# Optimization experiments

Measured on AMD Instinct MI355X. Metric: run time of the kernel, lower is better.

## Reference

```python
import jax, jax.numpy as jnp
import numpy as np

N, E, D, ED, SH = 100000, 1600000, 64, 16, 9

# Real spherical harmonics l=0,1,2, 'integral' normalization (e3nn default),
# applied to unit direction vectors. Coefficients: 1/(2*sqrt(pi)), sqrt(3/4pi), etc.

def _sh(d):
    x, y, z = d[:, 0], d[:, 1], d[:, 2]
    return jnp.stack([
        jnp.full_like(x, 0.28209479177387814),          # l=0
        0.4886025119029199 * y,                          # l=1, m=-1
        0.4886025119029199 * z,                          # l=1, m=0
        0.4886025119029199 * x,                          # l=1, m=1
        1.0925484305920792 * x * y,                      # l=2, m=-2
        1.0925484305920792 * y * z,                      # l=2, m=-1
        0.31539156525252005 * (3.0 * z * z - 1.0),       # l=2, m=0
        1.0925484305920792 * x * z,                      # l=2, m=1
        0.5462742152960396 * (x * x - y * y),            # l=2, m=2
    ], axis=1)


def _mlp(h, W1, b1, W2, b2):  # Linear -> SiLU -> Linear
    return jax.nn.silu(h @ W1 + b1) @ W2 + b2


def setup_inputs() -> dict:
    key = jax.random.key(0)
    ks = jax.random.split(key, 16)
    def rn(k, shape, scale=0.05):
        return jax.random.normal(k, shape, dtype=jnp.float32) * scale
    return {
        "x": jax.random.normal(ks[0], (N, D), jnp.float32),
        "pos": jax.random.normal(ks[1], (N, 3), jnp.float32) * 3.0,
        "edge_attr": jax.random.normal(ks[2], (E, ED), jnp.float32),
        "row": jax.random.randint(ks[3], (E,), 0, N, dtype=jnp.int32),
        "col": jax.random.randint(ks[4], (E,), 0, N, dtype=jnp.int32),
        "node_W1": rn(ks[5], (D, D)), "node_b1": jnp.zeros((D,), jnp.float32),
        "node_W2": rn(ks[6], (D, D)), "node_b2": jnp.zeros((D,), jnp.float32),
        "edge_W1": rn(ks[7], (SH + ED, D)), "edge_b1": jnp.zeros((D,), jnp.float32),
        "edge_W2": rn(ks[8], (D, D)), "edge_b2": jnp.zeros((D,), jnp.float32),
        "out_W1": rn(ks[9], (2 * D, D)), "out_b1": jnp.zeros((D,), jnp.float32),
        "out_W2": rn(ks[10], (D, D)), "out_b2": jnp.zeros((D,), jnp.float32),
        "bn_gamma": jnp.ones((D,), jnp.float32), "bn_beta": jnp.zeros((D,), jnp.float32),
    }


def reference(x, pos, edge_attr, row, col,
              node_W1, node_b1, node_W2, node_b2,
              edge_W1, edge_b1, edge_W2, edge_b2,
              out_W1, out_b1, out_W2, out_b2,
              bn_gamma, bn_beta):
    # gather node positions per edge -> relative vectors
    rel = pos[row] - pos[col]                                    # [E,3]
    length = jnp.sqrt(jnp.sum(rel * rel, axis=1, keepdims=True) + 1e-12)
    d = rel / length
    d = d / (jnp.sqrt(jnp.sum(d * d, axis=1, keepdims=True)) + 1e-10)
    edge_sh = _sh(d)                                             # [E,9]
    edge_feat = jnp.concatenate([edge_sh, edge_attr], axis=1)    # [E,9+ED]
    x_t = _mlp(x, node_W1, node_b1, node_W2, node_b2)            # [N,D]
    e_w = _mlp(edge_feat, edge_W1, edge_b1, edge_W2, edge_b2)    # [E,D]
    msg = x_t[row] * e_w                                         # message = x_j * edge_attr
    # scatter-mean onto target nodes (edge_index[1] == col)
    s = jax.ops.segment_sum(msg, col, num_segments=N)            # [N,D]
    cnt = jax.ops.segment_sum(jnp.ones((E,), msg.dtype), col, num_segments=N)
    agg = s / jnp.maximum(cnt, 1.0)[:, None]
    h = jnp.concatenate([agg, x], axis=1)                        # [N,2D]
    h = _mlp(h, out_W1, out_b1, out_W2, out_b2)                  # [N,D]
    # BatchNorm over node dim (scalar irreps), training-mode batch stats
    mean = jnp.mean(h, axis=0)
    var = jnp.var(h, axis=0)
    return (h - mean) / jnp.sqrt(var + 1e-5) * bn_gamma + bn_beta
```

## Files before the change

### kernel.cpp

```cpp
#include <hip/hip_runtime.h>
#include <math.h>

#define DD 64
#define EDA 16

#define FR_E1 0
#define FR_E2 4
#define FR_N1 12
#define FR_N2 20
#define FR_O1 28
#define FR_O2 44
#define FR_TOT 52

#define PADH 72
#define PADF 68

#define HS 72

typedef unsigned int u32;
typedef unsigned long long u64;
typedef __attribute__((ext_vector_type(8))) short short8;
typedef __attribute__((ext_vector_type(4))) float f32x4;

static __device__ __forceinline__ float silu(float v) {
    return v / (1.0f + __expf(-v));
}
static __device__ __forceinline__ unsigned short f2bf(float f) {
    unsigned u = __float_as_uint(f);
    unsigned r = u + 0x7FFFu + ((u >> 16) & 1u);
    return (unsigned short)(r >> 16);
}
static __device__ __forceinline__ float bf2f(unsigned short u) {
    return __uint_as_float(((unsigned)u) << 16);
}
static __device__ __forceinline__ float bflo(u32 v) {
    return __uint_as_float(v << 16);
}
static __device__ __forceinline__ float bfhi(u32 v) {
    return __uint_as_float(v & 0xFFFF0000u);
}
static __device__ __forceinline__ unsigned cvt_pk_bf16(float lo, float hi) {
    unsigned r;
    asm("v_cvt_pk_bf16_f32 %0, %1, %2" : "=v"(r) : "v"(lo), "v"(hi));
    return r;
}
static __device__ __forceinline__ int bperm(int idx_lane, int v) {
    return __builtin_amdgcn_ds_bpermute(idx_lane << 2, v);
}
static __device__ __forceinline__ void wave_lds_fence() {
    asm volatile("s_waitcnt lgkmcnt(0)" ::: "memory");
    __builtin_amdgcn_sched_barrier(0);
}

__global__ __launch_bounds__(256) void k_pack_zero(
    const float* __restrict__ eW1, const float* __restrict__ eW2,
    const float* __restrict__ nW1, const float* __restrict__ nW2,
    const float* __restrict__ oW1, const float* __restrict__ oW2,
    unsigned short* __restrict__ wpk,
    uint4* __restrict__ zbase, int nz4)
{
    if (blockIdx.x > 0) {
        int i = (blockIdx.x - 1) * 256 + threadIdx.x;
        if (i < nz4) zbase[i] = make_uint4(0u, 0u, 0u, 0u);
        return;
    }
    int t = threadIdx.x;
    int nt = t >> 6, l = t & 63;
    int kc = l >> 4, n0 = l & 15;

    #pragma unroll
    for (int j = 0; j < 8; ++j) {
        int k = kc*8 + j;
        int orig = (k < 16) ? (9 + k) : ((k < 25) ? (k - 16) : -1);
        float v = (orig >= 0) ? eW1[orig*DD + nt*16 + n0] : 0.0f;
        wpk[((size_t)((FR_E1 + nt)*64 + l))*8 + j] = f2bf(v);
    }
    #pragma unroll
    for (int s = 0; s < 2; ++s) {
        #pragma unroll
        for (int j = 0; j < 8; ++j) {
            int k = s*32 + kc*8 + j;
            wpk[((size_t)((FR_E2 + s*4 + nt)*64 + l))*8 + j] = f2bf(eW2[k*DD + nt*16 + n0]);
            wpk[((size_t)((FR_N1 + s*4 + nt)*64 + l))*8 + j] = f2bf(nW1[k*DD + nt*16 + n0]);
            wpk[((size_t)((FR_N2 + s*4 + nt)*64 + l))*8 + j] = f2bf(nW2[k*DD + nt*16 + n0]);
            wpk[((size_t)((FR_O2 + s*4 + nt)*64 + l))*8 + j] = f2bf(oW2[k*DD + nt*16 + n0]);
        }
    }
    #pragma unroll
    for (int s = 0; s < 4; ++s) {
        #pragma unroll
        for (int j = 0; j < 8; ++j) {
            int k = s*32 + kc*8 + j;
            wpk[((size_t)((FR_O1 + s*4 + nt)*64 + l))*8 + j] = f2bf(oW1[k*DD + nt*16 + n0]);
        }
    }
}

__global__ __launch_bounds__(256, 3) void k_node_hist(
    const float* __restrict__ x,
    const unsigned short* __restrict__ wpk,
    const float* __restrict__ b1, const float* __restrict__ b2,
    unsigned short* __restrict__ x_tb, int n, int nodeBlocks,
    const int* __restrict__ col, u32* __restrict__ cnt, int n_e)
{
    __shared__ __align__(16) unsigned short tile[4][16*PADH];
    const int tid  = threadIdx.x;

    if (blockIdx.x >= nodeBlocks) {
        int g = (blockIdx.x - nodeBlocks) * 256 + tid;
        int base = g * 4;
        if (base + 3 < n_e) {
            int4 c = ((const int4*)col)[g];
            atomicAdd(&cnt[c.x], 1u);
            atomicAdd(&cnt[c.y], 1u);
            atomicAdd(&cnt[c.z], 1u);
            atomicAdd(&cnt[c.w], 1u);
        } else {
            for (int e = base; e < n_e; ++e) atomicAdd(&cnt[col[e]], 1u);
        }
        return;
    }

    const int wv   = tid >> 6;
    const int lane = tid & 63;
    const int kc   = lane >> 4;
    const int n0   = lane & 15;
    const int rbase = kc * 4;

    const short8* fb = (const short8*)wpk;
    short8 bw1[2][4], bw2[2][4];
    #pragma unroll
    for (int s = 0; s < 2; ++s)
        #pragma unroll
        for (int nt = 0; nt < 4; ++nt) {
            bw1[s][nt] = fb[(FR_N1 + s*4 + nt)*64 + lane];
            bw2[s][nt] = fb[(FR_N2 + s*4 + nt)*64 + lane];
        }
    float b1v[4], b2v[4];
    #pragma unroll
    for (int nt = 0; nt < 4; ++nt) { b1v[nt] = b1[nt*16 + n0]; b2v[nt] = b2[nt*16 + n0]; }

    const int base = blockIdx.x*64 + wv*16;
    int rc = min(base + n0, n - 1);
    const float* xr = x + (size_t)rc * DD;

    short8 a[2];
    #pragma unroll
    for (int m = 0; m < 2; ++m) {
        float4 u0 = *(const float4*)(xr + m*32 + kc*8);
        float4 u1 = *(const float4*)(xr + m*32 + kc*8 + 4);
        unsigned* au = (unsigned*)&a[m];
        au[0] = cvt_pk_bf16(u0.x, u0.y);
        au[1] = cvt_pk_bf16(u0.z, u0.w);
        au[2] = cvt_pk_bf16(u1.x, u1.y);
        au[3] = cvt_pk_bf16(u1.z, u1.w);
    }

    f32x4 zz = {0.f, 0.f, 0.f, 0.f};
    f32x4 hacc[4] = {zz, zz, zz, zz};
    #pragma unroll
    for (int m = 0; m < 2; ++m)
        #pragma unroll
        for (int nt = 0; nt < 4; ++nt)
            hacc[nt] = __builtin_amdgcn_mfma_f32_16x16x32_bf16(a[m], bw1[m][nt], hacc[nt], 0, 0, 0);

    #pragma unroll
    for (int nt = 0; nt < 4; ++nt)
        #pragma unroll
        for (int r = 0; r < 4; ++r)
            tile[wv][(rbase + r)*PADH + nt*16 + n0] = f2bf(silu(hacc[nt][r] + b1v[nt]));
    __syncthreads();

    short8 a2_0 = *(const short8*)&tile[wv][n0*PADH +  0 + kc*8];
    short8 a2_1 = *(const short8*)&tile[wv][n0*PADH + 32 + kc*8];
    f32x4 oacc[4];
    #pragma unroll
    for (int nt = 0; nt < 4; ++nt) {
        oacc[nt] = __builtin_amdgcn_mfma_f32_16x16x32_bf16(a2_0, bw2[0][nt], zz, 0, 0, 0);
        oacc[nt] = __builtin_amdgcn_mfma_f32_16x16x32_bf16(a2_1, bw2[1][nt], oacc[nt], 0, 0, 0);
    }
    __syncthreads();

    #pragma unroll
    for (int nt = 0; nt < 4; ++nt)
        #pragma unroll
        for (int r = 0; r < 4; ++r)
            tile[wv][(rbase + r)*PADH + (n0>>2)*16 + nt*4 + (n0&3)] =
                f2bf(oacc[nt][r] + b2v[nt]);
    __syncthreads();

    int ei = lane >> 2, q = lane & 3;
    int er = base + ei;
    if (er < n) {
        uint4* dst = (uint4*)(x_tb + (size_t)er * DD);
        dst[q]     = *(const uint4*)&tile[wv][ei*PADH + q*8];
        dst[q + 4] = *(const uint4*)&tile[wv][ei*PADH + (q + 4)*8];
    }
}

__global__ __launch_bounds__(256) void k_scan_bump(
    const u32* __restrict__ cnt, u32* __restrict__ wp,
    u32* __restrict__ gctr, int n)
{
    __shared__ u32 s[256];
    __shared__ u32 base;
    int t = threadIdx.x;
    int i = blockIdx.x * 256 + t;
    u32 v = (i < n) ? cnt[i] : 0u;
    s[t] = v;
    __syncthreads();
    for (int o = 1; o < 256; o <<= 1) {
        u32 a = (t >= o) ? s[t - o] : 0u;
        __syncthreads();
        s[t] += a;
        __syncthreads();
    }
    if (t == 255) base = atomicAdd(gctr, s[255]);
    __syncthreads();
    if (i < n) wp[i] = base + s[t] - v;
}

__global__ __launch_bounds__(256) void k_scatter(
    const int* __restrict__ row, const int* __restrict__ col,
    u32* __restrict__ wp, u64* __restrict__ ce,
    float* __restrict__ agg, int n_agg4, int n_e)
{
    int e = blockIdx.x * 256 + threadIdx.x;
    if (e < n_agg4) {
        float4 z = {0.f, 0.f, 0.f, 0.f};
        ((float4*)agg)[e] = z;
    }
    if (e >= n_e) return;
    int c = col[e];
    int r = row[e];
    u32 p = atomicAdd(&wp[c], 1u);
    u32 lo = (u32)e | ((u32)r << 21);
    u32 hi = ((u32)r >> 11) | ((u32)c << 6);
    u64 pk = (u64)lo | ((u64)hi << 32);
    __builtin_nontemporal_store(pk, &ce[p]);
}

__global__ __launch_bounds__(256, 4) void k_edge_fused(
    const float* __restrict__ pos,
    const float* __restrict__ edge_attr,
    const u64* __restrict__ ce,
    const unsigned short* __restrict__ x_tb,
    const unsigned short* __restrict__ wpk,
    const float* __restrict__ b1, const float* __restrict__ b2,
    float* __restrict__ agg, int n_e)
{
    __shared__ __align__(16) unsigned short t_s[4][16*HS];
    __shared__ __align__(16) unsigned short wls[8*64*8];

    const int tid  = threadIdx.x;
    const int wv   = tid >> 6;
    const int lane = tid & 63;
    const int kc   = lane >> 4;
    const int n0   = lane & 15;

    {
        const uint4* wsrc = (const uint4*)(wpk + FR_E2*64*8);
        uint4* wdst = (uint4*)wls;
        wdst[tid*2]     = wsrc[tid*2];
        wdst[tid*2 + 1] = wsrc[tid*2 + 1];
    }

    const short8* fb = (const short8*)wpk;
    short8 bw1[4];
    #pragma unroll
    for (int nt = 0; nt < 4; ++nt) bw1[nt] = fb[(FR_E1 + nt)*64 + lane];

    uint2 bp1[4], bp2[4];
    #pragma unroll
    for (int nt = 0; nt < 4; ++nt) {
        float4 q1 = *(const float4*)(b1 + nt*16 + kc*4);
        float4 q2 = *(const float4*)(b2 + nt*16 + kc*4);
        bp1[nt].x = cvt_pk_bf16(q1.x, q1.y); bp1[nt].y = cvt_pk_bf16(q1.z, q1.w);
        bp2[nt].x = cvt_pk_bf16(q2.x, q2.y); bp2[nt].y = cvt_pk_bf16(q2.z, q2.w);
    }

    const int gbase = blockIdx.x*256 + wv*64;
    int g  = gbase + lane;
    int gc = min(g, n_e - 1);
    u64 pk = ce[gc];
    u32 pklo = (u32)pk, pkhi = (u32)(pk >> 32);
    int eo = (int)(pklo & 0x1FFFFFu);
    int rw = (int)((pklo >> 21) | ((pkhi & 0x3Fu) << 11));
    int cl = (int)(pkhi >> 6);

    float ax = pos[3*rw+0] - pos[3*cl+0];
    float ay = pos[3*rw+1] - pos[3*cl+1];
    float az = pos[3*rw+2] - pos[3*cl+2];
    float len = sqrtf(fmaf(ax,ax, fmaf(ay,ay, az*az)) + 1e-12f);
    float dx = ax/len, dy = ay/len, dz = az/len;
    float n2 = sqrtf(fmaf(dx,dx, fmaf(dy,dy, dz*dz)));
    float inv = 1.0f/(n2 + 1e-10f);
    dx *= inv; dy *= inv; dz *= inv;

    u32 shp01 = cvt_pk_bf16(0.28209479177387814f, 0.4886025119029199f*dy);
    u32 shp23 = cvt_pk_bf16(0.4886025119029199f*dz, 0.4886025119029199f*dx);
    u32 shp45 = cvt_pk_bf16(1.0925484305920792f*dx*dy, 1.0925484305920792f*dy*dz);
    u32 shp67 = cvt_pk_bf16(0.31539156525252005f*(3.0f*dz*dz - 1.0f),
                            1.0925484305920792f*dx*dz);
    u32 shp8  = cvt_pk_bf16(0.5462742152960396f*(dx*dx - dy*dy), 0.0f);

    int cln = bperm(min(lane + 1, 63), cl);
    u64 fmask = __ballot(cln != cl) | 0x8000800080008000ull;

    f32x4 zz = {0.f, 0.f, 0.f, 0.f};

    __syncthreads();

    #pragma unroll 1
    for (int tt = 0; tt < 4; ++tt) {
        const int le = tt*16 + n0;
        bool valid = (gbase + le) < n_e;

        int ea  = bperm(le, eo);
        int rv  = bperm(le, rw);
        u32 s01 = (u32)bperm(le, (int)shp01);
        u32 s23 = (u32)bperm(le, (int)shp23);
        u32 s45 = (u32)bperm(le, (int)shp45);
        u32 s67 = (u32)bperm(le, (int)shp67);
        u32 s8  = (u32)bperm(le, (int)shp8);

        const unsigned short* xrow = x_tb + (size_t)rv * DD + kc*16;
        uint4 qa = *(const uint4*)(xrow);
        uint4 qb = *(const uint4*)(xrow + 8);
        uint2 xv0 = {qa.x, qa.y}, xv1 = {qa.z, qa.w};
        uint2 xv2 = {qb.x, qb.y}, xv3 = {qb.z, qb.w};

        short8 af;
        unsigned* au = (unsigned*)&af;
        if (kc < 2) {
            const float4* ap = (const float4*)(edge_attr + (size_t)ea*EDA + kc*8);
            float4 a0 = ap[0], a1 = ap[1];
            au[0] = cvt_pk_bf16(a0.x, a0.y);
            au[1] = cvt_pk_bf16(a0.z, a0.w);
            au[2] = cvt_pk_bf16(a1.x, a1.y);
            au[3] = cvt_pk_bf16(a1.z, a1.w);
        } else if (kc == 2) {
            au[0] = s01; au[1] = s23; au[2] = s45; au[3] = s67;
        } else {
            au[0] = s8; au[1] = 0u; au[2] = 0u; au[3] = 0u;
        }

        f32x4 hacc[4];
        #pragma unroll
        for (int nt = 0; nt < 4; ++nt)
            hacc[nt] = __builtin_amdgcn_mfma_f32_16x16x32_bf16(bw1[nt], af, zz, 0, 0, 0);

        #pragma unroll
        for (int nt = 0; nt < 4; ++nt) {
            float h0 = silu(hacc[nt][0] + bflo(bp1[nt].x));
            float h1 = silu(hacc[nt][1] + bfhi(bp1[nt].x));
            float h2 = silu(hacc[nt][2] + bflo(bp1[nt].y));
            float h3 = silu(hacc[nt][3] + bfhi(bp1[nt].y));
            uint2 pr;
            pr.x = cvt_pk_bf16(h0, h1);
            pr.y = cvt_pk_bf16(h2, h3);
            *(uint2*)&t_s[wv][n0*HS + nt*16 + kc*4] = pr;
        }
        wave_lds_fence();

        short8 bf0 = *(const short8*)&t_s[wv][n0*HS +  0 + kc*8];
        short8 bf1 = *(const short8*)&t_s[wv][n0*HS + 32 + kc*8];
        f32x4 oacc[4];
        #pragma unroll
        for (int nt = 0; nt < 4; ++nt) {
            short8 w0 = *(const short8*)&wls[((0*4 + nt)*64 + lane)*8];
            oacc[nt] = __builtin_amdgcn_mfma_f32_16x16x32_bf16(w0, bf0, zz, 0, 0, 0);
            short8 w1 = *(const short8*)&wls[((1*4 + nt)*64 + lane)*8];
            oacc[nt] = __builtin_amdgcn_mfma_f32_16x16x32_bf16(w1, bf1, oacc[nt], 0, 0, 0);
        }

        if (!valid) {
            xv0.x = xv0.y = xv1.x = xv1.y = 0u;
            xv2.x = xv2.y = xv3.x = xv3.y = 0u;
        }
        {
            float m0, m1, m2, m3;
            uint2 pr;
            m0 = (oacc[0][0] + bflo(bp2[0].x)) * bflo(xv0.x);
            m1 = (oacc[0][1] + bfhi(bp2[0].x)) * bfhi(xv0.x);
            m2 = (oacc[0][2] + bflo(bp2[0].y)) * bflo(xv0.y);
            m3 = (oacc[0][3] + bfhi(bp2[0].y)) * bfhi(xv0.y);
            pr.x = cvt_pk_bf16(m0, m1); pr.y = cvt_pk_bf16(m2, m3);
            *(uint2*)&t_s[wv][n0*HS +  0 + kc*4] = pr;
            m0 = (oacc[1][0] + bflo(bp2[1].x)) * bflo(xv1.x);
            m1 = (oacc[1][1] + bfhi(bp2[1].x)) * bfhi(xv1.x);
            m2 = (oacc[1][2] + bflo(bp2[1].y)) * bflo(xv1.y);
            m3 = (oacc[1][3] + bfhi(bp2[1].y)) * bfhi(xv1.y);
            pr.x = cvt_pk_bf16(m0, m1); pr.y = cvt_pk_bf16(m2, m3);
            *(uint2*)&t_s[wv][n0*HS + 16 + kc*4] = pr;
            m0 = (oacc[2][0] + bflo(bp2[2].x)) * bflo(xv2.x);
            m1 = (oacc[2][1] + bfhi(bp2[2].x)) * bfhi(xv2.x);
            m2 = (oacc[2][2] + bflo(bp2[2].y)) * bflo(xv2.y);
            m3 = (oacc[2][3] + bfhi(bp2[2].y)) * bfhi(xv2.y);
            pr.x = cvt_pk_bf16(m0, m1); pr.y = cvt_pk_bf16(m2, m3);
            *(uint2*)&t_s[wv][n0*HS + 32 + kc*4] = pr;
            m0 = (oacc[3][0] + bflo(bp2[3].x)) * bflo(xv3.x);
            m1 = (oacc[3][1] + bfhi(bp2[3].x)) * bfhi(xv3.x);
            m2 = (oacc[3][2] + bflo(bp2[3].y)) * bflo(xv3.y);
            m3 = (oacc[3][3] + bfhi(bp2[3].y)) * bfhi(xv3.y);
            pr.x = cvt_pk_bf16(m0, m1); pr.y = cvt_pk_bf16(m2, m3);
            *(uint2*)&t_s[wv][n0*HS + 48 + kc*4] = pr;
        }
        wave_lds_fence();

        {
            float acc = 0.0f;
            #pragma unroll
            for (int r = 0; r < 16; ++r) {
                acc += bf2f(t_s[wv][r*HS + lane]);
                if ((fmask >> (tt*16 + r)) & 1ull) {
                    int cur = __builtin_amdgcn_readlane(cl, tt*16 + r);
                    unsafeAtomicAdd(&agg[(size_t)cur*DD + lane], acc);
                    acc = 0.0f;
                }
            }
        }
    }
}

__global__ __launch_bounds__(256, 2) void k_out_mfma(
    const float* __restrict__ agg, const u32* __restrict__ cnt,
    const float* __restrict__ x,
    const unsigned short* __restrict__ wpk,
    const float* __restrict__ b1, const float* __restrict__ b2,
    float* __restrict__ h, float* __restrict__ sums, int n)
{
    __shared__ __align__(16) unsigned short htile[4][16*PADH];
    __shared__ __align__(16) float otile[4][16*PADF];
    const int tid  = threadIdx.x;
    const int wv   = tid >> 6;
    const int lane = tid & 63;
    const int kc   = lane >> 4;
    const int n0   = lane & 15;
    const int rbase = kc * 4;

    const short8* fb = (const short8*)wpk;
    short8 bw1[4][4], bw2[2][4];
    #pragma unroll
    for (int s = 0; s < 4; ++s)
        #pragma unroll
        for (int nt = 0; nt < 4; ++nt) bw1[s][nt] = fb[(FR_O1 + s*4 + nt)*64 + lane];
    #pragma unroll
    for (int s = 0; s < 2; ++s)
        #pragma unroll
        for (int nt = 0; nt < 4; ++nt) bw2[s][nt] = fb[(FR_O2 + s*4 + nt)*64 + lane];

    float b1v[4], b2v[4];
    #pragma unroll
    for (int nt = 0; nt < 4; ++nt) { b1v[nt] = b1[nt*16 + n0]; b2v[nt] = b2[nt*16 + n0]; }

    const int base = blockIdx.x*64 + wv*16;
    int rc = min(base + n0, n - 1);
    const float* ar = agg + (size_t)rc * DD;
    const float* xr = x   + (size_t)rc * DD;
    float invc = 1.0f / fmaxf((float)cnt[rc], 1.0f);

    short8 a[4];
    #pragma unroll
    for (int m = 0; m < 4; ++m) {
        const float* src = (m < 2) ? (ar + m*32 + kc*8) : (xr + (m-2)*32 + kc*8);
        float4 u0 = *(const float4*)(src);
        float4 u1 = *(const float4*)(src + 4);
        if (m < 2) {
            u0.x*=invc; u0.y*=invc; u0.z*=invc; u0.w*=invc;
            u1.x*=invc; u1.y*=invc; u1.z*=invc; u1.w*=invc;
        }
        unsigned* au = (unsigned*)&a[m];
        au[0] = cvt_pk_bf16(u0.x, u0.y);
        au[1] = cvt_pk_bf16(u0.z, u0.w);
        au[2] = cvt_pk_bf16(u1.x, u1.y);
        au[3] = cvt_pk_bf16(u1.z, u1.w);
    }

    f32x4 zz = {0.f, 0.f, 0.f, 0.f};
    f32x4 hacc[4] = {zz, zz, zz, zz};
    #pragma unroll
    for (int m = 0; m < 4; ++m)
        #pragma unroll
        for (int nt = 0; nt < 4; ++nt)
            hacc[nt] = __builtin_amdgcn_mfma_f32_16x16x32_bf16(a[m], bw1[m][nt], hacc[nt], 0, 0, 0);

    #pragma unroll
    for (int nt = 0; nt < 4; ++nt)
        #pragma unroll
        for (int r = 0; r < 4; ++r)
            htile[wv][(rbase + r)*PADH + nt*16 + n0] = f2bf(silu(hacc[nt][r] + b1v[nt]));
    __syncthreads();

    short8 a2_0 = *(const short8*)&htile[wv][n0*PADH +  0 + kc*8];
    short8 a2_1 = *(const short8*)&htile[wv][n0*PADH + 32 + kc*8];
    f32x4 oacc[4];
    #pragma unroll
    for (int nt = 0; nt < 4; ++nt) {
        oacc[nt] = __builtin_amdgcn_mfma_f32_16x16x32_bf16(a2_0, bw2[0][nt], zz, 0, 0, 0);
        oacc[nt] = __builtin_amdgcn_mfma_f32_16x16x32_bf16(a2_1, bw2[1][nt], oacc[nt], 0, 0, 0);
    }

    #pragma unroll
    for (int nt = 0; nt < 4; ++nt)
        #pragma unroll
        for (int r = 0; r < 4; ++r)
            otile[wv][(rbase + r)*PADF + nt*16 + n0] = oacc[nt][r] + b2v[nt];
    __syncthreads();

    int ei = lane >> 2, q = lane & 3;
    int er = base + ei;
    if (er < n) {
        float4* dst = (float4*)(h + (size_t)er * DD);
        #pragma unroll
        for (int k = 0; k < 4; ++k)
            dst[q + 4*k] = *(const float4*)&otile[wv][ei*PADF + (q + 4*k)*4];
    }

    if (tid < 64) {
        int f = tid;
        float s = 0.f, qq = 0.f;
        #pragma unroll
        for (int w = 0; w < 4; ++w) {
            int base_w = blockIdx.x*64 + w*16;
            int nv = n - base_w;
            nv = nv < 0 ? 0 : (nv > 16 ? 16 : nv);
            for (int r = 0; r < nv; ++r) {
                float v = otile[w][r*PADF + f];
                s += v; qq = fmaf(v, v, qq);
            }
        }
        unsafeAtomicAdd(&sums[f], s);
        unsafeAtomicAdd(&sums[DD + f], qq);
    }
}

__global__ __launch_bounds__(256) void k_bn_norm(
    float* __restrict__ h, const float* __restrict__ sums,
    const float* __restrict__ gamma, const float* __restrict__ beta,
    float inv_n, int total4)
{
    int g = blockIdx.x*256 + threadIdx.x;
    if (g >= total4) return;
    int f0 = (g*4) & (DD-1);
    float4 v = ((const float4*)h)[g];
    float4 sm = *(const float4*)(sums + f0);
    float4 sq = *(const float4*)(sums + DD + f0);
    float4 gm = *(const float4*)(gamma + f0);
    float4 bt = *(const float4*)(beta + f0);
    float m0 = sm.x*inv_n, m1 = sm.y*inv_n, m2 = sm.z*inv_n, m3 = sm.w*inv_n;
    float s0 = gm.x * rsqrtf(sq.x*inv_n - m0*m0 + 1e-5f);
    float s1 = gm.y * rsqrtf(sq.y*inv_n - m1*m1 + 1e-5f);
    float s2 = gm.z * rsqrtf(sq.z*inv_n - m2*m2 + 1e-5f);
    float s3 = gm.w * rsqrtf(sq.w*inv_n - m3*m3 + 1e-5f);
    v.x = fmaf(v.x - m0, s0, bt.x);
    v.y = fmaf(v.y - m1, s1, bt.y);
    v.z = fmaf(v.z - m2, s2, bt.z);
    v.w = fmaf(v.w - m3, s3, bt.w);
    ((float4*)h)[g] = v;
}

static inline size_t al16(size_t v) { return (v + 15) & ~(size_t)15; }

extern "C" void kernel_launch(void* const* d_in, const int* in_sizes, int n_in,
                              void* d_out, int out_size, void* d_ws, size_t ws_size,
                              hipStream_t stream)
{
    const float* x         = (const float*)d_in[0];
    const float* pos       = (const float*)d_in[1];
    const float* edge_attr = (const float*)d_in[2];
    const int*   row       = (const int*)d_in[3];
    const int*   col       = (const int*)d_in[4];
    const float* nW1 = (const float*)d_in[5];
    const float* nb1 = (const float*)d_in[6];
    const float* nW2 = (const float*)d_in[7];
    const float* nb2 = (const float*)d_in[8];
    const float* eW1 = (const float*)d_in[9];
    const float* eb1 = (const float*)d_in[10];
    const float* eW2 = (const float*)d_in[11];
    const float* eb2 = (const float*)d_in[12];
    const float* oW1 = (const float*)d_in[13];
    const float* ob1 = (const float*)d_in[14];
    const float* oW2 = (const float*)d_in[15];
    const float* ob2 = (const float*)d_in[16];
    const float* gamma = (const float*)d_in[17];
    const float* beta  = (const float*)d_in[18];

    const int N = in_sizes[0] / DD;
    const int E = in_sizes[3];
    const int NB = (N + 255) / 256;
    const int nodeBlocks = (N + 63) / 64;
    const int histBlocks = (E/4 + 255) / 256;

    float* hout = (float*)d_out;
    char* ws = (char*)d_ws;

    size_t o_xtb  = 0;
    size_t o_cnt  = o_xtb  + (size_t)N*DD*2;
    size_t o_sums = o_cnt  + (size_t)N*4;
    size_t o_gctr = o_sums + 128*4;
    size_t o_agg  = o_gctr + 16;
    size_t o_wp   = o_agg  + (size_t)N*DD*4;
    size_t o_wpk  = al16(o_wp + (size_t)N*4);
    size_t o_ce   = al16(o_wpk + (size_t)FR_TOT*64*8*2);
    size_t need   = o_ce + (size_t)E*8;

    if (ws_size < need) return;

    unsigned short* x_tb = (unsigned short*)(ws + o_xtb);
    u32*   cnt  = (u32*)(ws + o_cnt);
    float* sums = (float*)(ws + o_sums);
    u32*   gctr = (u32*)(ws + o_gctr);
    float* agg  = (float*)(ws + o_agg);
    u32*   wp   = (u32*)(ws + o_wp);
    unsigned short* wpk = (unsigned short*)(ws + o_wpk);
    u64*   ce   = (u64*)(ws + o_ce);

    const int nz4 = (N + 132 + 3) / 4;
    const int zBlocks = (nz4 + 255) / 256;

    k_pack_zero<<<1 + zBlocks, 256, 0, stream>>>(eW1, eW2, nW1, nW2, oW1, oW2, wpk,
                                                 (uint4*)cnt, nz4);
    k_node_hist<<<nodeBlocks + histBlocks, 256, 0, stream>>>(
        x, wpk, nb1, nb2, x_tb, N, nodeBlocks, col, cnt, E);
    k_scan_bump<<<NB, 256, 0, stream>>>(cnt, wp, gctr, N);
    k_scatter<<<(E + 255)/256, 256, 0, stream>>>(row, col, wp, ce, agg, N*DD/4, E);
    k_edge_fused<<<(E + 255)/256, 256, 0, stream>>>(pos, edge_attr, ce, x_tb,
                                                    wpk, eb1, eb2, agg, E);
    k_out_mfma<<<(N + 63)/64, 256, 0, stream>>>(agg, cnt, x, wpk, ob1, ob2, hout, sums, N);
    k_bn_norm<<<(N*DD/4 + 255)/256, 256, 0, stream>>>(hout, sums, gamma, beta,
                                                      1.0f/(float)N, N*DD/4);
}
```

Measured before the change: 327.2 us.

## Permute edge_attr to sorted order as bf16 during scatter, read coalesced in edge kernel

The scatter kernel now reads each edge's attributes coalesced, converts them to bf16, and writes them into the destination-sorted slot. The fused edge kernel reads these contiguously by slot instead of gathering f32 attributes by original edge id. The packed edge record drops the edge index and stores row and col as plain 32-bit halves. This replaces a random 64-byte gather with streaming reads, at the cost of extra workspace and a scattered 32-byte write per edge in the scatter pass.

```diff
diff --git a/kernel.cpp b/kernel.cpp
--- a/kernel.cpp
+++ b/kernel.cpp
@@ -222,7 +222,9 @@
 
 __global__ __launch_bounds__(256) void k_scatter(
     const int* __restrict__ row, const int* __restrict__ col,
+    const float* __restrict__ edge_attr,
     u32* __restrict__ wp, u64* __restrict__ ce,
+    unsigned short* __restrict__ attr_s,
     float* __restrict__ agg, int n_agg4, int n_e)
 {
     int e = blockIdx.x * 256 + threadIdx.x;
@@ -234,15 +236,25 @@
     int c = col[e];
     int r = row[e];
     u32 p = atomicAdd(&wp[c], 1u);
-    u32 lo = (u32)e | ((u32)r << 21);
-    u32 hi = ((u32)r >> 11) | ((u32)c << 6);
-    u64 pk = (u64)lo | ((u64)hi << 32);
+    u64 pk = (u64)(u32)r | ((u64)(u32)c << 32);
     __builtin_nontemporal_store(pk, &ce[p]);
+
+    const float4* ap = (const float4*)(edge_attr + (size_t)e * EDA);
+    float4 a0 = ap[0], a1 = ap[1], a2 = ap[2], a3 = ap[3];
+    u64 w0 = (u64)cvt_pk_bf16(a0.x, a0.y) | ((u64)cvt_pk_bf16(a0.z, a0.w) << 32);
+    u64 w1 = (u64)cvt_pk_bf16(a1.x, a1.y) | ((u64)cvt_pk_bf16(a1.z, a1.w) << 32);
+    u64 w2 = (u64)cvt_pk_bf16(a2.x, a2.y) | ((u64)cvt_pk_bf16(a2.z, a2.w) << 32);
+    u64 w3 = (u64)cvt_pk_bf16(a3.x, a3.y) | ((u64)cvt_pk_bf16(a3.z, a3.w) << 32);
+    u64* dst = (u64*)(attr_s + (size_t)p * 16);
+    __builtin_nontemporal_store(w0, dst + 0);
+    __builtin_nontemporal_store(w1, dst + 1);
+    __builtin_nontemporal_store(w2, dst + 2);
+    __builtin_nontemporal_store(w3, dst + 3);
 }
 
 __global__ __launch_bounds__(256, 4) void k_edge_fused(
     const float* __restrict__ pos,
-    const float* __restrict__ edge_attr,
+    const unsigned short* __restrict__ attr_s,
     const u64* __restrict__ ce,
     const unsigned short* __restrict__ x_tb,
     const unsigned short* __restrict__ wpk,
@@ -283,10 +295,8 @@
     int g  = gbase + lane;
     int gc = min(g, n_e - 1);
     u64 pk = ce[gc];
-    u32 pklo = (u32)pk, pkhi = (u32)(pk >> 32);
-    int eo = (int)(pklo & 0x1FFFFFu);
-    int rw = (int)((pklo >> 21) | ((pkhi & 0x3Fu) << 11));
-    int cl = (int)(pkhi >> 6);
+    int rw = (int)(u32)pk;
+    int cl = (int)(u32)(pk >> 32);
 
     float ax = pos[3*rw+0] - pos[3*cl+0];
     float ay = pos[3*rw+1] - pos[3*cl+1];
@@ -316,7 +326,6 @@
         const int le = tt*16 + n0;
         bool valid = (gbase + le) < n_e;
 
-        int ea  = bperm(le, eo);
         int rv  = bperm(le, rw);
         u32 s01 = (u32)bperm(le, (int)shp01);
         u32 s23 = (u32)bperm(le, (int)shp23);
@@ -333,12 +342,9 @@
         short8 af;
         unsigned* au = (unsigned*)&af;
         if (kc < 2) {
-            const float4* ap = (const float4*)(edge_attr + (size_t)ea*EDA + kc*8);
-            float4 a0 = ap[0], a1 = ap[1];
-            au[0] = cvt_pk_bf16(a0.x, a0.y);
-            au[1] = cvt_pk_bf16(a0.z, a0.w);
-            au[2] = cvt_pk_bf16(a1.x, a1.y);
-            au[3] = cvt_pk_bf16(a1.z, a1.w);
+            int slot = min(gbase + le, n_e - 1);
+            uint4 av = *(const uint4*)(attr_s + (size_t)slot*16 + kc*8);
+            au[0] = av.x; au[1] = av.y; au[2] = av.z; au[3] = av.w;
         } else if (kc == 2) {
             au[0] = s01; au[1] = s23; au[2] = s45; au[3] = s67;
         } else {
@@ -603,7 +609,8 @@
     size_t o_wp   = o_agg  + (size_t)N*DD*4;
     size_t o_wpk  = al16(o_wp + (size_t)N*4);
     size_t o_ce   = al16(o_wpk + (size_t)FR_TOT*64*8*2);
-    size_t need   = o_ce + (size_t)E*8;
+    size_t o_att  = o_ce + (size_t)E*8;
+    size_t need   = o_att + (size_t)E*16*2;
 
     if (ws_size < need) return;
 
@@ -615,6 +622,7 @@
     u32*   wp   = (u32*)(ws + o_wp);
     unsigned short* wpk = (unsigned short*)(ws + o_wpk);
     u64*   ce   = (u64*)(ws + o_ce);
+    unsigned short* attr_s = (unsigned short*)(ws + o_att);
 
     const int nz4 = (N + 132 + 3) / 4;
     const int zBlocks = (nz4 + 255) / 256;
@@ -624,8 +632,9 @@
     k_node_hist<<<nodeBlocks + histBlocks, 256, 0, stream>>>(
         x, wpk, nb1, nb2, x_tb, N, nodeBlocks, col, cnt, E);
     k_scan_bump<<<NB, 256, 0, stream>>>(cnt, wp, gctr, N);
-    k_scatter<<<(E + 255)/256, 256, 0, stream>>>(row, col, wp, ce, agg, N*DD/4, E);
-    k_edge_fused<<<(E + 255)/256, 256, 0, stream>>>(pos, edge_attr, ce, x_tb,
+    k_scatter<<<(E + 255)/256, 256, 0, stream>>>(row, col, edge_attr, wp, ce, attr_s,
+                                                 agg, N*DD/4, E);
+    k_edge_fused<<<(E + 255)/256, 256, 0, stream>>>(pos, attr_s, ce, x_tb,
                                                     wpk, eb1, eb2, agg, E);
     k_out_mfma<<<(N + 63)/64, 256, 0, stream>>>(agg, cnt, x, wpk, ob1, ob2, hout, sums, N);
     k_bn_norm<<<(N*DD/4 + 255)/256, 256, 0, stream>>>(hout, sums, gamma, beta,
```

Result: slower. 434.0 us (+32.7%).
